# Kernel tuning notes

Hardware: AMD Instinct MI355X
Metric: run time of the kernel (lower is better)

## Reference

```python
import jax, jax.numpy as jnp
import numpy as np

CAPACITY = 8_388_608  # 2**23, power of two -> leftmost_leaf == capacity
N_UPDATES = 1_048_576  # 2**20


def setup_inputs() -> dict:
    key = jax.random.key(0)
    k1, k2, k3 = jax.random.split(key, 3)
    # Existing tree buffer; values[1] is root, values[CAPACITY:2*CAPACITY] are leaves.
    tree_values = jax.random.uniform(k1, (2 * CAPACITY,), dtype=jnp.float32)
    # Distinct leaf indices in [0, CAPACITY): torch scatter-assign with duplicate
    # indices is nondeterministic, so the meaningful case is distinct indices.
    indices = jax.random.permutation(k2, CAPACITY)[:N_UPDATES].astype(jnp.int32)
    values = jax.random.uniform(k3, (N_UPDATES,), dtype=jnp.float32)
    return {"tree_values": tree_values, "indices": indices, "values": values}


def reference(tree_values, indices, values):
    """SegmentTree.__setitem__ with op=add: set leaves, propagate sums to root.

    Returns the updated (2*capacity,) tree buffer.
    """
    capacity = tree_values.shape[0] // 2  # static python int
    depth = int(capacity).bit_length() - 1  # log2(capacity) levels to the root
    # _index_to_leaf: with power-of-two capacity, leaf = idx + capacity (no wrap).
    leaf = indices.astype(jnp.int32) + capacity
    tree = tree_values.at[leaf].set(values)
    idx = leaf
    # Original does torch.unique(idx//2) per level purely as an optimization;
    # duplicate parents recompute the identical value, so plain scatter-set of
    # op(left_child, right_child) is the same math and jit-friendly.
    for _ in range(depth):
        idx = idx // 2
        parent = tree[2 * idx] + tree[2 * idx + 1]
        tree = tree.at[idx].set(parent)
    return tree
```

## Files before the change

### kernel.cpp

```cpp
#include <hip/hip_runtime.h>


typedef unsigned int uint;
typedef unsigned char uchar;
typedef unsigned long long ull;

#define NBINS 1024
#define BCAP  2048

__device__ __forceinline__ ull pc64(ull c) {
    ull x = (c | (c >> 1)) & 0x5555555555555555ull;
    x = (x | (x >> 1))  & 0x3333333333333333ull;
    x = (x | (x >> 2))  & 0x0F0F0F0F0F0F0F0Full;
    x = (x | (x >> 4))  & 0x00FF00FF00FF00FFull;
    x = (x | (x >> 8))  & 0x0000FFFF0000FFFFull;
    x = (x | (x >> 16)) & 0x00000000FFFFFFFFull;
    return x;
}

__global__ __launch_bounds__(1024)
void bin_kernel(const int* __restrict__ idx,
                const float* __restrict__ val,
                uint* __restrict__ cnt,
                uint2* __restrict__ bins) {
    __shared__ uint hist[NBINS];
    __shared__ uint rbase[NBINS];
    const int tid = threadIdx.x;
    hist[tid] = 0u;
    __syncthreads();

    const int g = blockIdx.x * 1024 + tid;
    int4   j4 = ((const int4*)idx)[g];
    float4 v4 = ((const float4*)val)[g];
    uint  j[4] = { (uint)j4.x, (uint)j4.y, (uint)j4.z, (uint)j4.w };
    float v[4] = { v4.x, v4.y, v4.z, v4.w };

    #pragma unroll
    for (int e = 0; e < 4; ++e) atomicAdd(&hist[j[e] >> 13], 1u);
    __syncthreads();

    uint h = hist[tid];
    rbase[tid] = h ? atomicAdd(&cnt[tid], h) : 0u;
    hist[tid] = 0u;
    __syncthreads();

    #pragma unroll
    for (int e = 0; e < 4; ++e) {
        uint bin = j[e] >> 13;
        uint r = rbase[bin] + atomicAdd(&hist[bin], 1u);
        if (r < BCAP)
            bins[((size_t)bin << 11) + r] =
                make_uint2(j[e] & 8191u, __float_as_uint(v[e]));
    }
}

__global__ __launch_bounds__(1024)
void merge_kernel(const float* __restrict__ tree,
                  const uint* __restrict__ cnt,
                  const uint2* __restrict__ bins,
                  uint* __restrict__ l13v,
                  uint* __restrict__ l13f,
                  uint* __restrict__ done,
                  float* __restrict__ out, int C) {
    __shared__ float slv[8192];
    __shared__ uint  sflb[256];
    __shared__ float s9v[16];
    __shared__ uint  s9d[16];
    __shared__ uint  sticket;
    __shared__ float s16v[16];
    __shared__ uint  s16d[16];

    const int b    = blockIdx.x;
    const int tid  = threadIdx.x;
    const int wv   = tid >> 6;
    const int lane = tid & 63;
    const int r    = b * 16 + wv;
    const int leaf0  = tid * 8;
    const int gleaf0 = b * 8192 + leaf0;

    uint c = cnt[b];
    float4 ta = *(const float4*)(tree + C + gleaf0);
    float4 tb = *(const float4*)(tree + C + gleaf0 + 4);
    float4 t1 = *(const float4*)(tree + (C >> 1) + (gleaf0 >> 1));
    float2 t2 = *(const float2*)(tree + (C >> 2) + (gleaf0 >> 2));
    float t3v = tree[(C >> 3) + (gleaf0 >> 3)];
    float pt[6];
    #pragma unroll
    for (int lvl = 4; lvl <= 9; ++lvl) {
        int n = 64 >> (lvl - 3);
        pt[lvl - 4] = tree[(C >> lvl) + (r << (9 - lvl)) + (lane & (n - 1))];
    }
    float pu[4] = {0.f, 0.f, 0.f, 0.f};
    if (wv == 0) {
        #pragma unroll
        for (int lvl = 10; lvl <= 13; ++lvl) {
            int n = 1 << (13 - lvl);
            pu[lvl - 10] =
                tree[(C >> lvl) + (b << (13 - lvl)) + (lane & (n - 1))];
        }
    }

    if (tid < 256) sflb[tid] = 0u;
    __syncthreads();

    if (c > BCAP) c = BCAP;
    const uint2* mybin = bins + ((size_t)b << 11);
    for (uint k = tid; k < c; k += 1024u) {
        uint2 e = mybin[k];
        slv[e.x] = __uint_as_float(e.y);
        atomicOr(&sflb[e.x >> 5], 1u << (e.x & 31u));
    }
    __syncthreads();

    uint fw8 = (sflb[tid >> 2] >> ((tid & 3) * 8)) & 0xFFu;
    float4 la = *(const float4*)&slv[leaf0];
    float4 lb = *(const float4*)&slv[leaf0 + 4];

    float l0 = (fw8 &   1u) ? la.x : ta.x;
    float l1 = (fw8 &   2u) ? la.y : ta.y;
    float l2 = (fw8 &   4u) ? la.z : ta.z;
    float l3 = (fw8 &   8u) ? la.w : ta.w;
    float l4 = (fw8 &  16u) ? lb.x : tb.x;
    float l5 = (fw8 &  32u) ? lb.y : tb.y;
    float l6 = (fw8 &  64u) ? lb.z : tb.z;
    float l7 = (fw8 & 128u) ? lb.w : tb.w;

    *(float4*)(out + C + gleaf0)     = make_float4(l0, l1, l2, l3);
    *(float4*)(out + C + gleaf0 + 4) = make_float4(l4, l5, l6, l7);

    uint d10 = (fw8 &   3u) != 0u;
    uint d11 = (fw8 &  12u) != 0u;
    uint d12 = (fw8 &  48u) != 0u;
    uint d13 = (fw8 & 192u) != 0u;
    float4 v1;
    v1.x = d10 ? l0 + l1 : t1.x;
    v1.y = d11 ? l2 + l3 : t1.y;
    v1.z = d12 ? l4 + l5 : t1.z;
    v1.w = d13 ? l6 + l7 : t1.w;
    *(float4*)(out + (C >> 1) + (gleaf0 >> 1)) = v1;

    uint d20 = d10 | d11, d21 = d12 | d13;
    float2 v2;
    v2.x = d20 ? v1.x + v1.y : t2.x;
    v2.y = d21 ? v1.z + v1.w : t2.y;
    *(float2*)(out + (C >> 2) + (gleaf0 >> 2)) = v2;

    uint d3 = d20 | d21;
    float v = d3 ? v2.x + v2.y : t3v;
    out[(C >> 3) + (gleaf0 >> 3)] = v;

    ull m = __ballot(d3 != 0u);
    #pragma unroll
    for (int lvl = 4; lvl <= 9; ++lvl) {
        float a  = __shfl(v, 2 * lane, 64);
        float bb = __shfl(v, 2 * lane + 1, 64);
        m = pc64(m);
        int n = 64 >> (lvl - 3);
        if (lane < n) {
            int node = (C >> lvl) + (r << (9 - lvl)) + lane;
            uint dd = (uint)(m >> lane) & 1u;
            v = dd ? a + bb : pt[lvl - 4];
            out[node] = v;
        }
    }
    if (lane == 0) { s9v[wv] = v; s9d[wv] = (uint)(m & 1ull); }
    __syncthreads();

    if (wv == 0) {
        float vv = lane < 16 ? s9v[lane] : 0.f;
        uint dd  = lane < 16 ? s9d[lane] : 0u;
        ull mm = __ballot(dd != 0u);
        #pragma unroll
        for (int lvl = 10; lvl <= 13; ++lvl) {
            float a  = __shfl(vv, 2 * lane, 64);
            float bb = __shfl(vv, 2 * lane + 1, 64);
            mm = pc64(mm);
            int n = 1 << (13 - lvl);
            if (lane < n) {
                int node = (C >> lvl) + (b << (13 - lvl)) + lane;
                uint d2 = (uint)(mm >> lane) & 1u;
                vv = d2 ? a + bb : pu[lvl - 10];
                out[node] = vv;
            }
        }
        if (lane == 0) {
            uint o1 = atomicExch(&l13v[b], __float_as_uint(vv));
            uint o2 = atomicExch(&l13f[b], (uint)(mm & 1ull));
            asm volatile("" : : "v"(o1), "v"(o2));
            sticket = atomicAdd(done, 1u);
        }
    }
    __syncthreads();
    if (sticket != (uint)gridDim.x - 1u) return;

    {
        const int w2 = tid >> 6;
        float tv = __uint_as_float(atomicOr(&l13v[tid], 0u));
        uint  td = atomicOr(&l13f[tid], 0u);

        ull m2 = __ballot(td != 0u);
        #pragma unroll
        for (int M = 512; M >= 16; M >>= 1) {
            float a  = __shfl(tv, 2 * lane, 64);
            float bb = __shfl(tv, 2 * lane + 1, 64);
            m2 = pc64(m2);
            int nw = M >> 4;
            if (lane < nw) {
                int node = M + nw * w2 + lane;
                uint dd = (uint)(m2 >> lane) & 1u;
                tv = dd ? a + bb : tree[node];
                out[node] = tv;
            }
        }
        if (lane == 0) { s16v[w2] = tv; s16d[w2] = (uint)(m2 & 1ull); }
        __syncthreads();

        if (w2 == 0) {
            float vv2 = lane < 16 ? s16v[lane] : 0.f;
            uint dd2  = lane < 16 ? s16d[lane] : 0u;
            ull mm2 = __ballot(dd2 != 0u);
            #pragma unroll
            for (int M = 8; M >= 1; M >>= 1) {
                float a  = __shfl(vv2, 2 * lane, 64);
                float bb = __shfl(vv2, 2 * lane + 1, 64);
                mm2 = pc64(mm2);
                if (lane < M) {
                    uint d2 = (uint)(mm2 >> lane) & 1u;
                    vv2 = d2 ? a + bb : tree[M + lane];
                    out[M + lane] = vv2;
                }
            }
            if (lane == 0) out[0] = tree[0];
        }
    }
}

extern "C" void kernel_launch(void* const* d_in, const int* in_sizes, int n_in,
                              void* d_out, int out_size, void* d_ws, size_t ws_size,
                              hipStream_t stream) {
    const float* tree    = (const float*)d_in[0];
    const int*   indices = (const int*)d_in[1];
    const float* values  = (const float*)d_in[2];
    float* out = (float*)d_out;

    const int two_cap = in_sizes[0];
    const int C       = two_cap >> 1;
    const int nupd    = in_sizes[1];

    uchar* ws = (uchar*)d_ws;
    uint*  cnt  = (uint*)ws;
    uint*  done = (uint*)(ws + 4096);
    uint*  l13v = (uint*)(ws + 8192);
    uint*  l13f = (uint*)(ws + 12288);
    uint2* bins = (uint2*)(ws + 32768);

    (void)hipMemsetAsync(ws, 0, 4160, stream);
    bin_kernel<<<nupd / 4096, 1024, 0, stream>>>(indices, values, cnt, bins);
    merge_kernel<<<C / 8192, 1024, 0, stream>>>(tree, cnt, bins, l13v, l13f,
                                                done, out, C);
}
```

Baseline: 145.0 us.

## Halve merge block size to 4096 leaves with 2048 bins and 512 threads

Moves from 1024 bins of 8192 leaves to 2048 bins of 4096 leaves. The merge kernel now runs 2048 blocks of 512 threads instead of 1024 blocks of 1024 threads, and the final last-block reduction starts from level 12 and handles two extra levels per thread. The goal is more, smaller blocks for better occupancy and load balance. The cost is more global atomics on the bin counters and a longer serial tail in the last block. The bin capacity drops to 1024, which stays safe at the expected load of about 512 entries per bin.

```diff
diff --git a/kernel.cpp b/kernel.cpp
--- a/kernel.cpp
+++ b/kernel.cpp
@@ -5,8 +5,8 @@
 typedef unsigned char uchar;
 typedef unsigned long long ull;
 
-#define NBINS 1024
-#define BCAP  2048
+#define NBINS 2048
+#define BCAP  1024
 
 __device__ __forceinline__ ull pc64(ull c) {
     ull x = (c | (c >> 1)) & 0x5555555555555555ull;
@@ -27,6 +27,7 @@
     __shared__ uint rbase[NBINS];
     const int tid = threadIdx.x;
     hist[tid] = 0u;
+    hist[tid + 1024] = 0u;
     __syncthreads();
 
     const int g = blockIdx.x * 1024 + tid;
@@ -36,36 +37,40 @@
     float v[4] = { v4.x, v4.y, v4.z, v4.w };
 
     #pragma unroll
-    for (int e = 0; e < 4; ++e) atomicAdd(&hist[j[e] >> 13], 1u);
-    __syncthreads();
-
-    uint h = hist[tid];
-    rbase[tid] = h ? atomicAdd(&cnt[tid], h) : 0u;
-    hist[tid] = 0u;
+    for (int e = 0; e < 4; ++e) atomicAdd(&hist[j[e] >> 12], 1u);
+    __syncthreads();
+
+    #pragma unroll
+    for (int h2 = 0; h2 < 2; ++h2) {
+        int bin = h2 * 1024 + tid;
+        uint h = hist[bin];
+        rbase[bin] = h ? atomicAdd(&cnt[bin], h) : 0u;
+        hist[bin] = 0u;
+    }
     __syncthreads();
 
     #pragma unroll
     for (int e = 0; e < 4; ++e) {
-        uint bin = j[e] >> 13;
+        uint bin = j[e] >> 12;
         uint r = rbase[bin] + atomicAdd(&hist[bin], 1u);
         if (r < BCAP)
-            bins[((size_t)bin << 11) + r] =
-                make_uint2(j[e] & 8191u, __float_as_uint(v[e]));
-    }
-}
-
-__global__ __launch_bounds__(1024)
+            bins[((size_t)bin << 10) + r] =
+                make_uint2(j[e] & 4095u, __float_as_uint(v[e]));
+    }
+}
+
+__global__ __launch_bounds__(512)
 void merge_kernel(const float* __restrict__ tree,
                   const uint* __restrict__ cnt,
                   const uint2* __restrict__ bins,
-                  uint* __restrict__ l13v,
-                  uint* __restrict__ l13f,
+                  uint* __restrict__ l12v,
+                  uint* __restrict__ l12f,
                   uint* __restrict__ done,
                   float* __restrict__ out, int C) {
-    __shared__ float slv[8192];
-    __shared__ uint  sflb[256];
-    __shared__ float s9v[16];
-    __shared__ uint  s9d[16];
+    __shared__ float slv[4096];
+    __shared__ uint  sflb[128];
+    __shared__ float s9v[8];
+    __shared__ uint  s9d[8];
     __shared__ uint  sticket;
     __shared__ float s16v[16];
     __shared__ uint  s16d[16];
@@ -74,9 +79,9 @@
     const int tid  = threadIdx.x;
     const int wv   = tid >> 6;
     const int lane = tid & 63;
-    const int r    = b * 16 + wv;
+    const int r    = b * 8 + wv;
     const int leaf0  = tid * 8;
-    const int gleaf0 = b * 8192 + leaf0;
+    const int gleaf0 = b * 4096 + leaf0;
 
     uint c = cnt[b];
     float4 ta = *(const float4*)(tree + C + gleaf0);
@@ -90,22 +95,22 @@
         int n = 64 >> (lvl - 3);
         pt[lvl - 4] = tree[(C >> lvl) + (r << (9 - lvl)) + (lane & (n - 1))];
     }
-    float pu[4] = {0.f, 0.f, 0.f, 0.f};
+    float pu[3] = {0.f, 0.f, 0.f};
     if (wv == 0) {
         #pragma unroll
-        for (int lvl = 10; lvl <= 13; ++lvl) {
-            int n = 1 << (13 - lvl);
+        for (int lvl = 10; lvl <= 12; ++lvl) {
+            int n = 1 << (12 - lvl);
             pu[lvl - 10] =
-                tree[(C >> lvl) + (b << (13 - lvl)) + (lane & (n - 1))];
-        }
-    }
-
-    if (tid < 256) sflb[tid] = 0u;
+                tree[(C >> lvl) + (b << (12 - lvl)) + (lane & (n - 1))];
+        }
+    }
+
+    if (tid < 128) sflb[tid] = 0u;
     __syncthreads();
 
     if (c > BCAP) c = BCAP;
-    const uint2* mybin = bins + ((size_t)b << 11);
-    for (uint k = tid; k < c; k += 1024u) {
+    const uint2* mybin = bins + ((size_t)b << 10);
+    for (uint k = tid; k < c; k += 512u) {
         uint2 e = mybin[k];
         slv[e.x] = __uint_as_float(e.y);
         atomicOr(&sflb[e.x >> 5], 1u << (e.x & 31u));
@@ -167,25 +172,25 @@
     __syncthreads();
 
     if (wv == 0) {
-        float vv = lane < 16 ? s9v[lane] : 0.f;
-        uint dd  = lane < 16 ? s9d[lane] : 0u;
+        float vv = lane < 8 ? s9v[lane] : 0.f;
+        uint dd  = lane < 8 ? s9d[lane] : 0u;
         ull mm = __ballot(dd != 0u);
         #pragma unroll
-        for (int lvl = 10; lvl <= 13; ++lvl) {
+        for (int lvl = 10; lvl <= 12; ++lvl) {
             float a  = __shfl(vv, 2 * lane, 64);
             float bb = __shfl(vv, 2 * lane + 1, 64);
             mm = pc64(mm);
-            int n = 1 << (13 - lvl);
+            int n = 1 << (12 - lvl);
             if (lane < n) {
-                int node = (C >> lvl) + (b << (13 - lvl)) + lane;
+                int node = (C >> lvl) + (b << (12 - lvl)) + lane;
                 uint d2 = (uint)(mm >> lane) & 1u;
                 vv = d2 ? a + bb : pu[lvl - 10];
                 out[node] = vv;
             }
         }
         if (lane == 0) {
-            uint o1 = atomicExch(&l13v[b], __float_as_uint(vv));
-            uint o2 = atomicExch(&l13f[b], (uint)(mm & 1ull));
+            uint o1 = atomicExch(&l12v[b], __float_as_uint(vv));
+            uint o2 = atomicExch(&l12f[b], (uint)(mm & 1ull));
             asm volatile("" : : "v"(o1), "v"(o2));
             sticket = atomicAdd(done, 1u);
         }
@@ -195,16 +200,31 @@
 
     {
         const int w2 = tid >> 6;
-        float tv = __uint_as_float(atomicOr(&l13v[tid], 0u));
-        uint  td = atomicOr(&l13f[tid], 0u);
-
-        ull m2 = __ballot(td != 0u);
-        #pragma unroll
-        for (int M = 512; M >= 16; M >>= 1) {
+
+        float s12[4]; uint f12[4];
+        #pragma unroll
+        for (int k = 0; k < 4; ++k) {
+            s12[k] = __uint_as_float(atomicOr(&l12v[4 * tid + k], 0u));
+            f12[k] = atomicOr(&l12f[4 * tid + k], 0u);
+        }
+
+        float2 t13 = *(const float2*)(tree + 1024 + 2 * tid);
+        uint dA = f12[0] | f12[1], dB = f12[2] | f12[3];
+        float vA = dA ? s12[0] + s12[1] : t13.x;
+        float vB = dB ? s12[2] + s12[3] : t13.y;
+        *(float2*)(out + 1024 + 2 * tid) = make_float2(vA, vB);
+
+        uint d = dA | dB;
+        float tv = d ? vA + vB : tree[512 + tid];
+        out[512 + tid] = tv;
+
+        ull m2 = __ballot(d != 0u);
+        #pragma unroll
+        for (int M = 256; M >= 16; M >>= 1) {
             float a  = __shfl(tv, 2 * lane, 64);
             float bb = __shfl(tv, 2 * lane + 1, 64);
             m2 = pc64(m2);
-            int nw = M >> 4;
+            int nw = M >> 3;
             if (lane < nw) {
                 int node = M + nw * w2 + lane;
                 uint dd = (uint)(m2 >> lane) & 1u;
@@ -212,7 +232,8 @@
                 out[node] = tv;
             }
         }
-        if (lane == 0) { s16v[w2] = tv; s16d[w2] = (uint)(m2 & 1ull); }
+        if (lane < 2) { s16v[2 * w2 + lane] = tv;
+                        s16d[2 * w2 + lane] = (uint)(m2 >> lane) & 1u; }
         __syncthreads();
 
         if (w2 == 0) {
@@ -249,13 +270,13 @@
 
     uchar* ws = (uchar*)d_ws;
     uint*  cnt  = (uint*)ws;
-    uint*  done = (uint*)(ws + 4096);
-    uint*  l13v = (uint*)(ws + 8192);
-    uint*  l13f = (uint*)(ws + 12288);
+    uint*  done = (uint*)(ws + 8192);
+    uint*  l12v = (uint*)(ws + 12288);
+    uint*  l12f = (uint*)(ws + 20480);
     uint2* bins = (uint2*)(ws + 32768);
 
-    (void)hipMemsetAsync(ws, 0, 4160, stream);
+    (void)hipMemsetAsync(ws, 0, 8200, stream);
     bin_kernel<<<nupd / 4096, 1024, 0, stream>>>(indices, values, cnt, bins);
-    merge_kernel<<<C / 8192, 1024, 0, stream>>>(tree, cnt, bins, l13v, l13f,
-                                                done, out, C);
-}
+    merge_kernel<<<C / 4096, 512, 0, stream>>>(tree, cnt, bins, l12v, l12f,
+                                               done, out, C);
+}
```

After: 153.2 us. 5.7% more time.
